# Optimization experiments

Hardware: AMD Instinct MI355X
Metric: run time of the kernel (lower is better)

The kernel has to match this reference:

```python
import jax, jax.numpy as jnp
import numpy as np

IN_DIM = 128
OUT_DIM = 128
NUM_HEADS = 4
HEAD_DIM = OUT_DIM // NUM_HEADS  # 32
B, N = 4, 4096


def setup_inputs() -> dict:
    key = jax.random.key(0)
    ks = jax.random.split(key, 7)
    s_in = 1.0 / np.sqrt(IN_DIM)
    s_out = 1.0 / np.sqrt(OUT_DIM)
    return {
        "x": jax.random.normal(ks[0], (B, N, IN_DIM), dtype=jnp.float32),
        "adjacency": jax.random.randint(ks[1], (N, N), 0, 2, dtype=jnp.int32),
        "W_q": jax.random.uniform(ks[2], (IN_DIM, NUM_HEADS * HEAD_DIM), jnp.float32, -s_in, s_in),
        "W_k": jax.random.uniform(ks[3], (IN_DIM, NUM_HEADS * HEAD_DIM), jnp.float32, -s_in, s_in),
        "W_v": jax.random.uniform(ks[4], (IN_DIM, NUM_HEADS * HEAD_DIM), jnp.float32, -s_in, s_in),
        "W_o": jax.random.uniform(ks[5], (OUT_DIM, OUT_DIM), jnp.float32, -s_out, s_out),
        "b_o": jax.random.uniform(ks[6], (OUT_DIM,), jnp.float32, -s_out, s_out),
    }


def reference(x, adjacency, W_q, W_k, W_v, W_o, b_o):
    Bn, Nn, _ = x.shape
    # QKV projections -> (B, H, N, Dh)
    q = (x @ W_q).reshape(Bn, Nn, NUM_HEADS, HEAD_DIM).transpose(0, 2, 1, 3)
    k = (x @ W_k).reshape(Bn, Nn, NUM_HEADS, HEAD_DIM).transpose(0, 2, 1, 3)
    v = (x @ W_v).reshape(Bn, Nn, NUM_HEADS, HEAD_DIM).transpose(0, 2, 1, 3)
    scores = jnp.einsum("bhnd,bhmd->bhnm", q, k) / np.sqrt(HEAD_DIM).astype(np.float32)
    # adjacency mask (1,1,N,N): -inf where no edge
    adj = adjacency[None, None, :, :]
    scores = jnp.where(adj == 0, -jnp.inf, scores)
    attn = jax.nn.softmax(scores, axis=-1)
    out = jnp.einsum("bhnm,bhmd->bhnd", attn, v)
    out = out.transpose(0, 2, 1, 3).reshape(Bn, Nn, NUM_HEADS * HEAD_DIM)  # concat heads
    return out @ W_o + b_o
```

## Files before the change

### kernel.cpp

```cpp
#include <hip/hip_runtime.h>
#include <stdint.h>

typedef __attribute__((ext_vector_type(4))) short short4v;
typedef __attribute__((ext_vector_type(8))) short bf16x8;
typedef __attribute__((ext_vector_type(4))) float f32x4;
typedef __attribute__((ext_vector_type(2))) uint32_t uint2v;
typedef __attribute__((ext_vector_type(4))) uint32_t uint4v;
typedef __attribute__((ext_vector_type(4))) uint16_t ushort4v;

#define NN 4096

__device__ __forceinline__ uint16_t f2bf(float f) {
    union { float f; uint32_t u; } c; c.f = f;
    uint32_t r = c.u + 0x7FFF + ((c.u >> 16) & 1);
    return (uint16_t)(r >> 16);
}

__global__ __launch_bounds__(256) void wpack_kernel(
    const float* __restrict__ Wq, const float* __restrict__ Wk,
    const float* __restrict__ Wv, const float* __restrict__ Wo,
    uint16_t* __restrict__ WT, uint16_t* __restrict__ WoT)
{
    const int t = blockIdx.x * 256 + threadIdx.x;
    if (t < 3 * 128 * 128) {
        int j = t >> 7, k = t & 127;
        int m = j >> 7, jj = j & 127;
        const float* W = (m == 0) ? Wq : ((m == 1) ? Wk : Wv);
        float v = W[k * 128 + jj];
        if (m == 0) v *= (0.17677669529663687f * 1.4426950408889634f);
        WT[t] = f2bf(v);
    } else {
        int t2 = t - 3 * 128 * 128;
        int j = t2 >> 7, k = t2 & 127;
        WoT[t2] = f2bf(Wo[k * 128 + j]);
    }
}

__global__ __launch_bounds__(256) void adjqkv_kernel(
    const int* __restrict__ adj, uint64_t* __restrict__ bits,
    const float* __restrict__ x, const uint16_t* __restrict__ WT,
    uint16_t* __restrict__ Q, uint16_t* __restrict__ Kf, uint16_t* __restrict__ Vf)
{
    const int blk = blockIdx.x;
    const int tid = threadIdx.x;
    const int wave = tid >> 6, lane = tid & 63;

    if (blk >= 768) {
        const int ablk = blk - 768;
        const int wid = (ablk * 256 + tid) >> 6;
        const int base = wid * 32;
        const int* src = adj + (size_t)base * 64 + lane;
#pragma unroll 1
        for (int ii = 0; ii < 32; ii += 4) {
            int v0 = src[(ii + 0) * 64];
            int v1 = src[(ii + 1) * 64];
            int v2 = src[(ii + 2) * 64];
            int v3 = src[(ii + 3) * 64];
            uint64_t m0 = __ballot(v0 != 0);
            uint64_t m1 = __ballot(v1 != 0);
            uint64_t m2 = __ballot(v2 != 0);
            uint64_t m3 = __ballot(v3 != 0);
            if (lane == 0) {
                bits[base + ii + 0] = m0;
                bits[base + ii + 1] = m1;
                bits[base + ii + 2] = m2;
                bits[base + ii + 3] = m3;
            }
        }
        return;
    }

    const int g = lane >> 4, l15 = lane & 15;
    const int m = blk >> 8;
    const int ntile = (blk & 255) * 4 + wave;
    const int n = ntile * 16 + l15;
    const int b = n >> 12, nn = n & 4095;

    const char* xrow = (const char*)x + (size_t)n * 512;
    bf16x8 xb[4];
#pragma unroll
    for (int ks = 0; ks < 4; ++ks) {
        f32x4 a = *(const f32x4*)(xrow + ks * 128 + g * 16);
        f32x4 c = *(const f32x4*)(xrow + ks * 128 + 64 + g * 16);
        bf16x8 f;
#pragma unroll
        for (int i = 0; i < 4; ++i) { f[i] = (short)f2bf(a[i]); f[4 + i] = (short)f2bf(c[i]); }
        xb[ks] = f;
    }

#pragma unroll 1
    for (int jt = m * 8; jt < m * 8 + 8; ++jt) {
        const int j0 = jt * 16;
        const bool isV = (m == 2);
        const char* wrow = (const char*)WT + (size_t)(j0 + l15) * 256;
        f32x4 acc = {0.f, 0.f, 0.f, 0.f};
#pragma unroll
        for (int ks = 0; ks < 4; ++ks) {
            short4v a0 = *(const short4v*)(wrow + ks * 64 + g * 8);
            short4v a1 = *(const short4v*)(wrow + ks * 64 + 32 + g * 8);
            bf16x8 af = __builtin_shufflevector(a0, a1, 0, 1, 2, 3, 4, 5, 6, 7);
            acc = isV ? __builtin_amdgcn_mfma_f32_16x16x32_bf16(xb[ks], af, acc, 0, 0, 0)
                      : __builtin_amdgcn_mfma_f32_16x16x32_bf16(af, xb[ks], acc, 0, 0, 0);
        }
        const int bh = b * 4 + ((j0 & 127) >> 5);
        const int half = (j0 >> 4) & 1;
        ushort4v st;
#pragma unroll
        for (int r = 0; r < 4; ++r) st[r] = f2bf(acc[r]);
        if (m == 0) {
            const int d0 = (j0 & 31) + g * 4;
            *(ushort4v*)(Q + ((size_t)bh * 4096 + nn) * 32 + d0) = st;
        } else if (m == 1) {
            *(ushort4v*)(Kf + ((size_t)bh << 17) + (ntile & 255) * 512 + lane * 8 + half * 4) = st;
        } else {
            *(ushort4v*)(Vf + ((size_t)bh << 17) + ((ntile & 255) >> 1) * 1024
                         + half * 512 + lane * 8 + ((ntile & 1) << 2)) = st;
        }
    }
}

__global__ __launch_bounds__(256) void attn_kernel(
    const uint16_t* __restrict__ Q, const uint16_t* __restrict__ Kf,
    const uint16_t* __restrict__ Vf, const uint32_t* __restrict__ bits,
    uint16_t* __restrict__ O)
{
    __shared__ f32x4 cmb[4][4][2][64];
    __shared__ float csum[4][4][64];
    const int tid = threadIdx.x;
    const int wave = tid >> 6, lane = tid & 63;
    const int g = lane >> 4, l15 = lane & 15, gsh = g * 4;
    const int blk = blockIdx.x;
    const int bh = ((blk & 7) << 1) | ((blk >> 3) & 1);
    const int qb = blk >> 4;
    const int q0 = qb * 64;

    const char* Kp = (const char*)Kf + ((size_t)bh << 18) + wave * 65536 + lane * 16;
    const char* Vp = (const char*)Vf + ((size_t)bh << 18) + wave * 65536 + lane * 16;
    const uint32_t* ap[4];
#pragma unroll
    for (int qg = 0; qg < 4; ++qg)
        ap[qg] = bits + (size_t)(q0 + qg * 16 + l15) * 128 + wave * 32;

    bf16x8 qf[4];
#pragma unroll
    for (int qg = 0; qg < 4; ++qg) {
        const char* qrow = (const char*)Q + ((size_t)bh * 4096 + q0 + qg * 16 + l15) * 64;
        short4v a0 = *(const short4v*)(qrow + g * 8);
        short4v a1 = *(const short4v*)(qrow + 32 + g * 8);
        qf[qg] = __builtin_shufflevector(a0, a1, 0, 1, 2, 3, 4, 5, 6, 7);
    }

    bf16x8 ones;
#pragma unroll
    for (int i = 0; i < 8; ++i) ones[i] = (short)0x3F80;

    const f32x4 z = {0.f, 0.f, 0.f, 0.f};
    f32x4 o[4][2], sacc[4];
#pragma unroll
    for (int qg = 0; qg < 4; ++qg) { o[qg][0] = z; o[qg][1] = z; sacc[qg] = z; }

    bf16x8 kc[4], kn[4];
    uint2v wc[4], wn[4];
#pragma unroll
    for (int j = 0; j < 4; ++j) kc[j] = *(const bf16x8*)(Kp + j * 1024);
    Kp += 4096;
#pragma unroll
    for (int qg = 0; qg < 4; ++qg) { wc[qg] = *(const uint2v*)ap[qg]; ap[qg] += 2; }

    auto body = [&](bf16x8 (&kcur)[4], uint2v (&wcur)[4],
                    bf16x8 (&knxt)[4], uint2v (&wnxt)[4]) {
#pragma unroll
        for (int j = 0; j < 4; ++j) knxt[j] = *(const bf16x8*)(Kp + j * 1024);
        Kp += 4096;
#pragma unroll
        for (int qg = 0; qg < 4; ++qg) { wnxt[qg] = *(const uint2v*)ap[qg]; ap[qg] += 2; }
        bf16x8 vc[4];
#pragma unroll
        for (int i = 0; i < 4; ++i) vc[i] = *(const bf16x8*)(Vp + i * 1024);
        Vp += 4096;

#pragma unroll
        for (int qg = 0; qg < 4; ++qg) {
            f32x4 s[4];
            __builtin_amdgcn_s_setprio(1);
#pragma unroll
            for (int j = 0; j < 4; ++j)
                s[j] = __builtin_amdgcn_mfma_f32_16x16x32_bf16(kcur[j], qf[qg], z, 0, 0, 0);
            __builtin_amdgcn_s_setprio(0);
            float p[16];
#pragma unroll
            for (int j = 0; j < 4; ++j) {
                uint32_t wj = wcur[qg][j >> 1] >> (((j & 1) << 4) + gsh);
#pragma unroll
                for (int r = 0; r < 4; ++r) {
                    float pv = __builtin_amdgcn_exp2f(s[j][r]);
                    int msk = ((int)(wj << (31 - r))) >> 31;
                    p[j * 4 + r] = __uint_as_float(__float_as_uint(pv) & (uint32_t)msk);
                }
            }
            uint32_t pk[8];
#pragma unroll
            for (int i = 0; i < 8; ++i) {
                uint32_t r_;
                asm("v_cvt_pk_bf16_f32 %0, %1, %2" : "=v"(r_) : "v"(p[2 * i]), "v"(p[2 * i + 1]));
                pk[i] = r_;
            }
            uint4v u0 = {pk[0], pk[1], pk[2], pk[3]};
            uint4v u1 = {pk[4], pk[5], pk[6], pk[7]};
            bf16x8 pf0 = __builtin_bit_cast(bf16x8, u0);
            bf16x8 pf1 = __builtin_bit_cast(bf16x8, u1);
            __builtin_amdgcn_s_setprio(1);
            o[qg][0] = __builtin_amdgcn_mfma_f32_16x16x32_bf16(vc[0], pf0, o[qg][0], 0, 0, 0);
            o[qg][0] = __builtin_amdgcn_mfma_f32_16x16x32_bf16(vc[2], pf1, o[qg][0], 0, 0, 0);
            o[qg][1] = __builtin_amdgcn_mfma_f32_16x16x32_bf16(vc[1], pf0, o[qg][1], 0, 0, 0);
            o[qg][1] = __builtin_amdgcn_mfma_f32_16x16x32_bf16(vc[3], pf1, o[qg][1], 0, 0, 0);
            sacc[qg] = __builtin_amdgcn_mfma_f32_16x16x32_bf16(ones, pf0, sacc[qg], 0, 0, 0);
            sacc[qg] = __builtin_amdgcn_mfma_f32_16x16x32_bf16(ones, pf1, sacc[qg], 0, 0, 0);
            __builtin_amdgcn_s_setprio(0);
        }
    };

#pragma unroll 1
    for (int tt = 0; tt < 16; tt += 2) {
        body(kc, wc, kn, wn);
        body(kn, wn, kc, wc);
    }

#pragma unroll
    for (int qg = 0; qg < 4; ++qg) {
        cmb[wave][qg][0][lane] = o[qg][0];
        cmb[wave][qg][1][lane] = o[qg][1];
        csum[wave][qg][lane] = sacc[qg][0];
    }
    __syncthreads();
    {
        const int qg = wave;
        f32x4 a0 = cmb[0][qg][0][lane];
        f32x4 a1 = cmb[0][qg][1][lane];
        float sd = csum[0][qg][lane];
#pragma unroll
        for (int v = 1; v < 4; ++v) {
            a0 += cmb[v][qg][0][lane];
            a1 += cmb[v][qg][1][lane];
            sd += csum[v][qg][lane];
        }
        const float inv = 1.0f / sd;
        const int q = q0 + qg * 16 + l15;
        uint16_t* orow = O + ((size_t)bh * 4096 + q) * 32;
        ushort4v st0, st1;
#pragma unroll
        for (int r = 0; r < 4; ++r) {
            st0[r] = f2bf(a0[r] * inv);
            st1[r] = f2bf(a1[r] * inv);
        }
        *(ushort4v*)(orow + gsh) = st0;
        *(ushort4v*)(orow + 16 + gsh) = st1;
    }
}

__global__ __launch_bounds__(256) void proj_kernel(
    const uint16_t* __restrict__ A, const uint16_t* __restrict__ WoT,
    const float* __restrict__ bo, float* __restrict__ out)
{
    const int wave = threadIdx.x >> 6, lane = threadIdx.x & 63;
    const int g = lane >> 4, l15 = lane & 15;
    const int blk = blockIdx.x;
    const int ctbase = (blk >> 8) * 2;
    const int ntile = (blk & 255) * 4 + wave;
    const int n = ntile * 16 + l15;
    const int b = n >> 12, nn = n & 4095;

    bf16x8 bfr[4];
#pragma unroll
    for (int h = 0; h < 4; ++h) {
        const char* arow = (const char*)A + (((size_t)(b * 4 + h)) * 4096 + nn) * 64;
        short4v a0 = *(const short4v*)(arow + g * 8);
        short4v a1 = *(const short4v*)(arow + 32 + g * 8);
        bfr[h] = __builtin_shufflevector(a0, a1, 0, 1, 2, 3, 4, 5, 6, 7);
    }
#pragma unroll 1
    for (int ct = ctbase; ct < ctbase + 2; ++ct) {
        const int c0 = ct * 16;
        const char* wrow = (const char*)WoT + (size_t)(c0 + l15) * 256;
        f32x4 acc = {0.f, 0.f, 0.f, 0.f};
#pragma unroll
        for (int h = 0; h < 4; ++h) {
            short4v a0 = *(const short4v*)(wrow + h * 64 + g * 8);
            short4v a1 = *(const short4v*)(wrow + h * 64 + 32 + g * 8);
            bf16x8 af = __builtin_shufflevector(a0, a1, 0, 1, 2, 3, 4, 5, 6, 7);
            acc = __builtin_amdgcn_mfma_f32_16x16x32_bf16(af, bfr[h], acc, 0, 0, 0);
        }
        f32x4 bias = *(const f32x4*)(bo + c0 + g * 4);
#pragma unroll
        for (int r = 0; r < 4; ++r) acc[r] += bias[r];
        *(f32x4*)(out + (size_t)n * 128 + c0 + g * 4) = acc;
    }
}

extern "C" void kernel_launch(void* const* d_in, const int* in_sizes, int n_in,
                              void* d_out, int out_size, void* d_ws, size_t ws_size,
                              hipStream_t stream)
{
    const float* x   = (const float*)d_in[0];
    const int*   adj = (const int*)d_in[1];
    const float* Wq  = (const float*)d_in[2];
    const float* Wk  = (const float*)d_in[3];
    const float* Wv  = (const float*)d_in[4];
    const float* Wo  = (const float*)d_in[5];
    const float* bo  = (const float*)d_in[6];
    float* out = (float*)d_out;

    char* ws = (char*)d_ws;
    uint16_t* Q    = (uint16_t*)(ws);
    uint16_t* Kf   = (uint16_t*)(ws + ((size_t)4 << 20));
    uint16_t* Vf   = (uint16_t*)(ws + ((size_t)8 << 20));
    uint16_t* AO   = (uint16_t*)(ws + ((size_t)12 << 20));
    uint32_t* bits = (uint32_t*)(ws + ((size_t)16 << 20));
    uint16_t* WT   = (uint16_t*)(ws + ((size_t)18 << 20));
    uint16_t* WoT  = (uint16_t*)(ws + ((size_t)18 << 20) + 98304);

    hipLaunchKernelGGL(wpack_kernel, dim3(256), dim3(256), 0, stream,
                       Wq, Wk, Wv, Wo, WT, WoT);
    hipLaunchKernelGGL(adjqkv_kernel, dim3(2816), dim3(256), 0, stream,
                       adj, (uint64_t*)bits, x, WT, Q, Kf, Vf);
    hipLaunchKernelGGL(attn_kernel, dim3(1024), dim3(256), 0, stream,
                       Q, Kf, Vf, bits, AO);
    hipLaunchKernelGGL(proj_kernel, dim3(1024), dim3(256), 0, stream,
                       AO, WoT, bo, out);
}
```

Baseline: 123.3 us.

## Transpose adjacency bitmask to word-major layout and drop setprio hints in attention

The packed adjacency bitmask is now stored transposed, with each 32-bit word index major and query rows contiguous. The attention kernel's mask loads therefore coalesce across the 16 query lanes instead of striding by 512 bytes. The pointer-increment K/V/mask prefetch is replaced with index-based addressing and a guard on the final prefetch, and the s_setprio hints around the MFMAs are removed. In exchange, the packing kernel now does scattered 4-byte stores from lane 0, and dropping setprio may change how waves interleave.

```diff
diff --git a/kernel.cpp b/kernel.cpp
--- a/kernel.cpp
+++ b/kernel.cpp
@@ -37,7 +37,7 @@
 }
 
 __global__ __launch_bounds__(256) void adjqkv_kernel(
-    const int* __restrict__ adj, uint64_t* __restrict__ bits,
+    const int* __restrict__ adj, uint32_t* __restrict__ bitsT32,
     const float* __restrict__ x, const uint16_t* __restrict__ WT,
     uint16_t* __restrict__ Q, uint16_t* __restrict__ Kf, uint16_t* __restrict__ Vf)
 {
@@ -49,6 +49,8 @@
         const int ablk = blk - 768;
         const int wid = (ablk * 256 + tid) >> 6;
         const int base = wid * 32;
+        const int row = base >> 6;
+        const int w64b = base & 63;
         const int* src = adj + (size_t)base * 64 + lane;
 #pragma unroll 1
         for (int ii = 0; ii < 32; ii += 4) {
@@ -61,10 +63,15 @@
             uint64_t m2 = __ballot(v2 != 0);
             uint64_t m3 = __ballot(v3 != 0);
             if (lane == 0) {
-                bits[base + ii + 0] = m0;
-                bits[base + ii + 1] = m1;
-                bits[base + ii + 2] = m2;
-                bits[base + ii + 3] = m3;
+                const int w0 = (w64b + ii) * 2;
+                bitsT32[(size_t)(w0 + 0) * 4096 + row] = (uint32_t)m0;
+                bitsT32[(size_t)(w0 + 1) * 4096 + row] = (uint32_t)(m0 >> 32);
+                bitsT32[(size_t)(w0 + 2) * 4096 + row] = (uint32_t)m1;
+                bitsT32[(size_t)(w0 + 3) * 4096 + row] = (uint32_t)(m1 >> 32);
+                bitsT32[(size_t)(w0 + 4) * 4096 + row] = (uint32_t)m2;
+                bitsT32[(size_t)(w0 + 5) * 4096 + row] = (uint32_t)(m2 >> 32);
+                bitsT32[(size_t)(w0 + 6) * 4096 + row] = (uint32_t)m3;
+                bitsT32[(size_t)(w0 + 7) * 4096 + row] = (uint32_t)(m3 >> 32);
             }
         }
         return;
@@ -121,7 +128,7 @@
 
 __global__ __launch_bounds__(256) void attn_kernel(
     const uint16_t* __restrict__ Q, const uint16_t* __restrict__ Kf,
-    const uint16_t* __restrict__ Vf, const uint32_t* __restrict__ bits,
+    const uint16_t* __restrict__ Vf, const uint32_t* __restrict__ bitsT32,
     uint16_t* __restrict__ O)
 {
     __shared__ f32x4 cmb[4][4][2][64];
@@ -134,12 +141,12 @@
     const int qb = blk >> 4;
     const int q0 = qb * 64;
 
-    const char* Kp = (const char*)Kf + ((size_t)bh << 18) + wave * 65536 + lane * 16;
-    const char* Vp = (const char*)Vf + ((size_t)bh << 18) + wave * 65536 + lane * 16;
-    const uint32_t* ap[4];
+    const char* Kbase = (const char*)Kf + ((size_t)bh << 18) + wave * 65536 + lane * 16;
+    const char* Vbase = (const char*)Vf + ((size_t)bh << 18) + wave * 65536 + lane * 16;
+    const uint32_t* mb[4];
 #pragma unroll
     for (int qg = 0; qg < 4; ++qg)
-        ap[qg] = bits + (size_t)(q0 + qg * 16 + l15) * 128 + wave * 32;
+        mb[qg] = bitsT32 + (size_t)(wave * 32) * 4096 + (q0 + qg * 16 + l15);
 
     bf16x8 qf[4];
 #pragma unroll
@@ -162,31 +169,36 @@
     bf16x8 kc[4], kn[4];
     uint2v wc[4], wn[4];
 #pragma unroll
-    for (int j = 0; j < 4; ++j) kc[j] = *(const bf16x8*)(Kp + j * 1024);
-    Kp += 4096;
-#pragma unroll
-    for (int qg = 0; qg < 4; ++qg) { wc[qg] = *(const uint2v*)ap[qg]; ap[qg] += 2; }
-
-    auto body = [&](bf16x8 (&kcur)[4], uint2v (&wcur)[4],
+    for (int j = 0; j < 4; ++j) kc[j] = *(const bf16x8*)(Kbase + j * 1024);
+#pragma unroll
+    for (int qg = 0; qg < 4; ++qg) {
+        wc[qg][0] = mb[qg][0];
+        wc[qg][1] = mb[qg][4096];
+    }
+
+    auto body = [&](int tcur, int tnxt, bf16x8 (&kcur)[4], uint2v (&wcur)[4],
                     bf16x8 (&knxt)[4], uint2v (&wnxt)[4]) {
-#pragma unroll
-        for (int j = 0; j < 4; ++j) knxt[j] = *(const bf16x8*)(Kp + j * 1024);
-        Kp += 4096;
-#pragma unroll
-        for (int qg = 0; qg < 4; ++qg) { wnxt[qg] = *(const uint2v*)ap[qg]; ap[qg] += 2; }
+        if (tnxt < 16) {
+#pragma unroll
+            for (int j = 0; j < 4; ++j)
+                knxt[j] = *(const bf16x8*)(Kbase + (size_t)tnxt * 4096 + j * 1024);
+#pragma unroll
+            for (int qg = 0; qg < 4; ++qg) {
+                wnxt[qg][0] = mb[qg][(size_t)(2 * tnxt) * 4096];
+                wnxt[qg][1] = mb[qg][(size_t)(2 * tnxt + 1) * 4096];
+            }
+        }
         bf16x8 vc[4];
 #pragma unroll
-        for (int i = 0; i < 4; ++i) vc[i] = *(const bf16x8*)(Vp + i * 1024);
-        Vp += 4096;
+        for (int i = 0; i < 4; ++i)
+            vc[i] = *(const bf16x8*)(Vbase + (size_t)tcur * 4096 + i * 1024);
 
 #pragma unroll
         for (int qg = 0; qg < 4; ++qg) {
             f32x4 s[4];
-            __builtin_amdgcn_s_setprio(1);
 #pragma unroll
             for (int j = 0; j < 4; ++j)
                 s[j] = __builtin_amdgcn_mfma_f32_16x16x32_bf16(kcur[j], qf[qg], z, 0, 0, 0);
-            __builtin_amdgcn_s_setprio(0);
             float p[16];
 #pragma unroll
             for (int j = 0; j < 4; ++j) {
@@ -209,21 +221,19 @@
             uint4v u1 = {pk[4], pk[5], pk[6], pk[7]};
             bf16x8 pf0 = __builtin_bit_cast(bf16x8, u0);
             bf16x8 pf1 = __builtin_bit_cast(bf16x8, u1);
-            __builtin_amdgcn_s_setprio(1);
             o[qg][0] = __builtin_amdgcn_mfma_f32_16x16x32_bf16(vc[0], pf0, o[qg][0], 0, 0, 0);
             o[qg][0] = __builtin_amdgcn_mfma_f32_16x16x32_bf16(vc[2], pf1, o[qg][0], 0, 0, 0);
             o[qg][1] = __builtin_amdgcn_mfma_f32_16x16x32_bf16(vc[1], pf0, o[qg][1], 0, 0, 0);
             o[qg][1] = __builtin_amdgcn_mfma_f32_16x16x32_bf16(vc[3], pf1, o[qg][1], 0, 0, 0);
             sacc[qg] = __builtin_amdgcn_mfma_f32_16x16x32_bf16(ones, pf0, sacc[qg], 0, 0, 0);
             sacc[qg] = __builtin_amdgcn_mfma_f32_16x16x32_bf16(ones, pf1, sacc[qg], 0, 0, 0);
-            __builtin_amdgcn_s_setprio(0);
         }
     };
 
 #pragma unroll 1
     for (int tt = 0; tt < 16; tt += 2) {
-        body(kc, wc, kn, wn);
-        body(kn, wn, kc, wc);
+        body(tt, tt + 1, kc, wc, kn, wn);
+        body(tt + 1, tt + 2, kn, wn, kc, wc);
     }
 
 #pragma unroll
@@ -311,20 +321,20 @@
     float* out = (float*)d_out;
 
     char* ws = (char*)d_ws;
-    uint16_t* Q    = (uint16_t*)(ws);
-    uint16_t* Kf   = (uint16_t*)(ws + ((size_t)4 << 20));
-    uint16_t* Vf   = (uint16_t*)(ws + ((size_t)8 << 20));
-    uint16_t* AO   = (uint16_t*)(ws + ((size_t)12 << 20));
-    uint32_t* bits = (uint32_t*)(ws + ((size_t)16 << 20));
-    uint16_t* WT   = (uint16_t*)(ws + ((size_t)18 << 20));
-    uint16_t* WoT  = (uint16_t*)(ws + ((size_t)18 << 20) + 98304);
+    uint16_t* Q      = (uint16_t*)(ws);
+    uint16_t* Kf     = (uint16_t*)(ws + ((size_t)4 << 20));
+    uint16_t* Vf     = (uint16_t*)(ws + ((size_t)8 << 20));
+    uint16_t* AO     = (uint16_t*)(ws + ((size_t)12 << 20));
+    uint32_t* bitsT32= (uint32_t*)(ws + ((size_t)16 << 20));
+    uint16_t* WT     = (uint16_t*)(ws + ((size_t)18 << 20));
+    uint16_t* WoT    = (uint16_t*)(ws + ((size_t)18 << 20) + 98304);
 
     hipLaunchKernelGGL(wpack_kernel, dim3(256), dim3(256), 0, stream,
                        Wq, Wk, Wv, Wo, WT, WoT);
     hipLaunchKernelGGL(adjqkv_kernel, dim3(2816), dim3(256), 0, stream,
-                       adj, (uint64_t*)bits, x, WT, Q, Kf, Vf);
+                       adj, bitsT32, x, WT, Q, Kf, Vf);
     hipLaunchKernelGGL(attn_kernel, dim3(1024), dim3(256), 0, stream,
-                       Q, Kf, Vf, bits, AO);
+                       Q, Kf, Vf, bitsT32, AO);
     hipLaunchKernelGGL(proj_kernel, dim3(1024), dim3(256), 0, stream,
                        AO, WoT, bo, out);
 }
```

Result: faster. 120.8 us (median of 2 runs) (-2.1%).
